# Optimization experiments

Measured on AMD Instinct MI355X. Metric: run time of the kernel, lower is better.

## Reference

```python
import jax, jax.numpy as jnp
import numpy as np

N_FFT = 1024
HOP = 256


def _hann(n):
    # torch.hann_window default is periodic
    return 0.5 * (1.0 - jnp.cos(2.0 * jnp.pi * jnp.arange(n) / n))


def _dft_kernel():
    # rfft(eye(n_fft)).T -> (n_fft//2+1, n_fft) complex, windowed along time axis
    win = _hann(N_FFT).astype(jnp.float32)
    dftm = jnp.fft.rfft(jnp.eye(N_FFT, dtype=jnp.float32), axis=-1).T * win[None, :]
    # rearrange 'f n ri -> (ri f) n': real rows first, then imag rows
    ker = jnp.concatenate([dftm.real, dftm.imag], axis=0)  # (2*(n_fft//2+1), n_fft)
    f2 = ker.shape[0]
    scale = jnp.ones((f2,), dtype=jnp.float32)
    scale = scale.at[1:(N_FFT + 1) // 2].set(2.0)   # positive freqs (real part), excl. DC & Nyquist
    scale = scale.at[(N_FFT + 2) // 2:].set(2.0)    # imag rows
    return (ker * scale[:, None] / N_FFT).astype(jnp.float32)  # (1026, 1024)


def setup_inputs() -> dict:
    key = jax.random.key(0)
    B, F, T = 16, N_FFT // 2 + 1, 1024
    x = jax.random.normal(key, (B, F, T, 2), dtype=jnp.float32)
    return {"x": x}


def reference(x) -> jnp.ndarray:
    # x: (B, freq, n_frames, 2)
    B, F, T, _ = x.shape
    # '... freq n ri -> ... (ri freq) n'
    xc = jnp.concatenate([x[..., 0], x[..., 1]], axis=1)  # (B, 2F, T)
    ker = _dft_kernel()                                   # (2F, n_fft)
    # conv_transpose1d(stride=hop) == per-frame GEMM then overlap-add
    frames = jnp.einsum('bct,cn->btn', xc, ker)           # (B, T, n_fft)
    L = (T - 1) * HOP + N_FFT
    idx = (jnp.arange(T)[:, None] * HOP + jnp.arange(N_FFT)[None, :]).reshape(-1)
    wav = jnp.zeros((B, L), dtype=x.dtype).at[:, idx].add(frames.reshape(B, -1))
    # COLA normalization: * hop / sum(window^2)
    win = _hann(N_FFT)
    coeff = (HOP / jnp.sum(win ** 2)).astype(x.dtype)
    return wav * coeff
```

## Files before the change

### kernel.cpp

```cpp
#include <hip/hip_runtime.h>
#include <hip/hip_bf16.h>

#define HOP 256
#define NB 16
#define NT 1024
#define MM (NB*NT)
#define LOUT ((NT-1)*HOP + 1024)
#define CQ (2.0f/(3.0f*1024.0f))
#define PACK_BLOCKS 2048

typedef __bf16 bf16x8 __attribute__((ext_vector_type(8)));
typedef float f32x4 __attribute__((ext_vector_type(4)));

__device__ __forceinline__ void gload_lds16(const void* g, void* l) {
  __builtin_amdgcn_global_load_lds(
      (const __attribute__((address_space(1))) void*)g,
      (__attribute__((address_space(3))) void*)l, 16, 0, 0);
}

__global__ void prep(const float* __restrict__ x, __hip_bfloat16* __restrict__ A,
                     __hip_bfloat16* __restrict__ B3, float* __restrict__ wint) {
  int tid = threadIdx.x;
  if (blockIdx.x >= PACK_BLOCKS) {
    int idx = (blockIdx.x - PACK_BLOCKS) * 256 + tid;
    int row = idx >> 9, c = idx & 511;
    int i = row & 255, nt = row >> 8;
    int oddh = i >> 7;
    int j = nt * 128 + (i & 127);
    int f, isSin;
    if (!oddh) {
      if (c < 257) { f = 2 * c; isSin = 0; } else { f = 2 * (c - 256); isSin = 1; }
    } else {
      if (c < 256) { f = 2 * c + 1; isSin = 0; } else { f = 2 * (c - 256) + 1; isSin = 1; }
    }
    const float w0 = 6.283185307179586f / 1024.f;
    int ph = (f * j) & 1023;
    float si, co;
    __sincosf((float)ph * w0, &si, &co);
    float sc = (f == 0 || f == 512) ? 1.f : 2.f;
    B3[idx] = __float2bfloat16(isSin ? -si * sc : co * sc);
    if (idx < 1024)
      wint[idx] = (0.5f - 0.5f * __cosf((float)idx * w0)) * CQ;
    return;
  }
  __shared__ float2 tile[64][65];
  int w = blockIdx.x;
  int b = w >> 7, fy = (w >> 4) & 7, tx = w & 15;
  int f0 = fy * 64, t0 = tx * 64;
  int tl = tid & 63, th = tid >> 6;
#pragma unroll
  for (int r = 0; r < 16; ++r) {
    int fl = r * 4 + th;
    tile[fl][tl] = *(const float2*)(x + (((size_t)b * 513 + f0 + fl) * 1024 + (t0 + tl)) * 2);
  }
  __syncthreads();
  int row = tid >> 2, s = tid & 3;
  float sp = 0.f;
  if (fy == 0 && s == 1)
    sp = x[(((size_t)b * 513 + 512) * 1024 + t0 + row) * 2];
  int cbase = (s & 1) * 256 + (s >> 1) * 512 + f0 / 2;
#pragma unroll
  for (int v = 0; v < 4; ++v) {
    bf16x8 pv;
#pragma unroll
    for (int u = 0; u < 8; ++u) {
      int e = v * 8 + u;
      float2 tv = tile[2 * e + (s >> 1)][row];
      float val = (s & 1) ? tv.y : tv.x;
      if (fy == 0 && s == 1 && e == 0) val = sp;
      pv[u] = (__bf16)val;
    }
    *(bf16x8*)(A + (size_t)(b * 1024 + t0 + row) * 1024 + cbase + v * 8) = pv;
  }
}

__global__ __launch_bounds__(256, 2) void gemm8(
    const __hip_bfloat16* __restrict__ A, const __hip_bfloat16* __restrict__ B3,
    const float* __restrict__ wint, __hip_bfloat16* __restrict__ C) {
  __shared__ __align__(16) __hip_bfloat16 smem[32768];
  int tid = threadIdx.x, lane = tid & 63, wv = tid >> 6;
  int wr = wv >> 1, wc = wv & 1;
  int q = blockIdx.x >> 3, xcd = blockIdx.x & 7;
  int m_ = xcd + 8 * (q >> 2);
  int nt = q & 3;
  int M0 = m_ * 128;
  int j0 = nt * 128;

  __hip_bfloat16* sA0 = smem;
  __hip_bfloat16* sA1 = smem + 8192;
  __hip_bfloat16* sB0 = smem + 16384;
  __hip_bfloat16* sB1 = smem + 24576;

  f32x4 accE[4][4] = {};
  f32x4 accO[4][4] = {};

#define SGA(KT, G, LB)                                                         \
  {                                                                            \
    int r_ = (G) * 32 + (tid >> 3);                                            \
    int s_ = (((tid & 7) ^ (r_ & 7)) * 8);                                     \
    gload_lds16(A + (size_t)(M0 + r_) * 1024 + (KT) * 64 + s_,                 \
                (LB) + (G) * 2048 + tid * 8);                                  \
  }
#define SGB(KT, G, LB)                                                         \
  {                                                                            \
    int r_ = (G) * 32 + (tid >> 3);                                            \
    int s_ = (((tid & 7) ^ (r_ & 7)) * 8);                                     \
    gload_lds16(B3 + (size_t)(nt * 256 + ((KT) >= 8 ? 128 : 0) + r_) * 512 +   \
                    ((KT) & 7) * 64 + s_,                                      \
                (LB) + (G) * 2048 + tid * 8);                                  \
  }
#define VMCNT0() asm volatile("s_waitcnt vmcnt(0)" ::: "memory")
#define BAR() __builtin_amdgcn_s_barrier()

#define TILE(CA, CB, NA, NBUF, K1, DOST, ACC)                                  \
  {                                                                            \
    if (DOST) { SGB(K1, 0, NBUF); SGB(K1, 1, NBUF);                            \
                SGB(K1, 2, NBUF); SGB(K1, 3, NBUF);                            \
                SGA(K1, 0, NA); SGA(K1, 1, NA);                                \
                SGA(K1, 2, NA); SGA(K1, 3, NA); }                              \
    bf16x8 bfr[2][4], af[4][2];                                                \
    _Pragma("unroll") for (int ni = 0; ni < 4; ++ni) {                         \
      int row = wc * 64 + ni * 16 + (lane & 15);                               \
      _Pragma("unroll") for (int ks = 0; ks < 2; ++ks)                         \
          bfr[ks][ni] = *(const bf16x8*)&(CB)[row * 64 +                       \
              (((ks * 4 + (lane >> 4)) ^ (row & 7)) * 8)];                     \
    }                                                                          \
    _Pragma("unroll") for (int mi = 0; mi < 4; ++mi) {                         \
      int row = wr * 64 + mi * 16 + (lane & 15);                               \
      _Pragma("unroll") for (int ks = 0; ks < 2; ++ks)                         \
          af[mi][ks] = *(const bf16x8*)&(CA)[row * 64 +                        \
              (((ks * 4 + (lane >> 4)) ^ (row & 7)) * 8)];                     \
    }                                                                          \
    __builtin_amdgcn_s_setprio(1);                                             \
    _Pragma("unroll") for (int mi = 0; mi < 4; ++mi)                           \
    _Pragma("unroll") for (int ks = 0; ks < 2; ++ks)                           \
    _Pragma("unroll") for (int ni = 0; ni < 4; ++ni)                           \
        ACC[mi][ni] = __builtin_amdgcn_mfma_f32_16x16x32_bf16(                 \
            af[mi][ks], bfr[ks][ni], ACC[mi][ni], 0, 0, 0);                    \
    __builtin_amdgcn_s_setprio(0);                                             \
    VMCNT0();                                                                  \
    BAR();                                                                     \
  }

  SGB(0, 0, sB0); SGB(0, 1, sB0); SGB(0, 2, sB0); SGB(0, 3, sB0);
  SGA(0, 0, sA0); SGA(0, 1, sA0); SGA(0, 2, sA0); SGA(0, 3, sA0);
  VMCNT0();
  BAR();

#pragma unroll
  for (int tt = 0; tt < 4; ++tt) {
    TILE(sA0, sB0, sA1, sB1, 2 * tt + 1, 1, accE);
    TILE(sA1, sB1, sA0, sB0, 2 * tt + 2, 1, accE);
  }
#pragma unroll
  for (int tt = 0; tt < 4; ++tt) {
    TILE(sA0, sB0, sA1, sB1, 2 * tt + 9, 1, accO);
    TILE(sA1, sB1, sA0, sB0, 2 * tt + 10, (tt < 3) ? 1 : 0, accO);
  }

  __hip_bfloat16* ct = smem;
  float wE[4], wO[4];
#pragma unroll
  for (int ni = 0; ni < 4; ++ni) {
    int jcol = j0 + wc * 64 + ni * 16 + (lane & 15);
    wE[ni] = wint[jcol];
    wO[ni] = wint[jcol + 512];
  }
#pragma unroll
  for (int mi = 0; mi < 4; ++mi) {
    int rbase = wr * 64 + mi * 16 + (lane >> 4) * 4;
#pragma unroll
    for (int ni = 0; ni < 4; ++ni) {
      int lc = wc * 64 + ni * 16 + (lane & 15);
#pragma unroll
      for (int r = 0; r < 4; ++r) {
        float E = accE[mi][ni][r], O = accO[mi][ni][r];
        ct[(rbase + r) * 256 + lc] = __float2bfloat16(wE[ni] * (E + O));
        ct[(rbase + r) * 256 + 128 + lc] = __float2bfloat16(wO[ni] * (E - O));
      }
    }
  }
  BAR();
#pragma unroll
  for (int k = 0; k < 16; ++k) {
    int row = k * 8 + (tid >> 5);
    int c0 = (tid & 31) * 8;
    int gcol = (c0 < 128) ? (j0 + c0) : (512 + j0 + c0 - 128);
    *(int4*)(C + (size_t)(M0 + row) * 1024 + gcol) = *(const int4*)&ct[row * 256 + c0];
  }
#undef SGA
#undef SGB
#undef VMCNT0
#undef BAR
#undef TILE
}

__global__ void ola2(const __hip_bfloat16* __restrict__ C, float* __restrict__ out) {
  int q = blockIdx.x;
  int b = blockIdx.y * 8 + (threadIdx.x >> 5);
  int r0 = (threadIdx.x & 31) * 8;
  size_t outl = (size_t)b * LOUT + q * 256 + r0;
  if (q >= 3 && q < 1024) {
    size_t mrow = ((size_t)b * 1024 + q) * 1024;
    bf16x8 v0 = *(const bf16x8*)&C[mrow + r0];
    bf16x8 v1 = *(const bf16x8*)&C[mrow - 1024 + 256 + r0];
    bf16x8 v2 = *(const bf16x8*)&C[mrow - 2048 + 512 + r0];
    bf16x8 v3 = *(const bf16x8*)&C[mrow - 3072 + 768 + r0];
    float res[8];
#pragma unroll
    for (int e = 0; e < 8; ++e)
      res[e] = (float)v0[e] + (float)v1[e] + (float)v2[e] + (float)v3[e];
    *(float4*)(out + outl) = make_float4(res[0], res[1], res[2], res[3]);
    *(float4*)(out + outl + 4) = make_float4(res[4], res[5], res[6], res[7]);
    return;
  }
#pragma unroll
  for (int e = 0; e < 8; ++e) {
    int l = q * 256 + r0 + e;
    int thi = l >> 8; if (thi > 1023) thi = 1023;
    int tlo = (l - 768) >> 8; if (tlo < 0) tlo = 0;
    float s = 0.f;
    for (int t = tlo; t <= thi; ++t)
      s += __bfloat162float(C[((size_t)b * 1024 + t) * 1024 + (l - (t << 8))]);
    out[outl + e] = s;
  }
}

extern "C" void kernel_launch(void* const* d_in, const int* in_sizes, int n_in,
                              void* d_out, int out_size, void* d_ws, size_t ws_size,
                              hipStream_t stream) {
  (void)in_sizes; (void)n_in; (void)out_size; (void)ws_size;
  const float* x = (const float*)d_in[0];
  float* out = (float*)d_out;
  char* ws = (char*)d_ws;
  size_t oA  = 0;
  size_t oB3 = oA + (size_t)MM * 1024 * 2;
  size_t oW  = oB3 + (size_t)1024 * 512 * 2;
  size_t oC  = oW + 1024 * 4;
  __hip_bfloat16* A  = (__hip_bfloat16*)(ws + oA);
  __hip_bfloat16* B3 = (__hip_bfloat16*)(ws + oB3);
  float* wint = (float*)(ws + oW);
  __hip_bfloat16* C  = (__hip_bfloat16*)(ws + oC);

  prep<<<dim3(PACK_BLOCKS + 2048), dim3(256), 0, stream>>>(x, A, B3, wint);
  gemm8<<<dim3(512), dim3(256), 0, stream>>>(A, B3, wint, C);
  ola2<<<dim3(1027, 2), dim3(256), 0, stream>>>(C, out);
}
```

Measured before the change: 59.45 us.

## Load B operand fragments directly from global into registers, bypassing LDS

The B (DFT kernel) tile is no longer staged through shared memory. Each wave now loads its bf16x8 MFMA fragments straight from global memory into a double-buffered register set, one tile ahead. This halves LDS traffic and removes the LDS reads for B. In exchange it adds register pressure from the second B fragment set, and each of the two column waves issues its own uncoalesced-ish global loads for the same B rows that the block previously loaded once.

```diff
diff --git a/kernel.cpp b/kernel.cpp
--- a/kernel.cpp
+++ b/kernel.cpp
@@ -88,11 +88,10 @@
 
   __hip_bfloat16* sA0 = smem;
   __hip_bfloat16* sA1 = smem + 8192;
-  __hip_bfloat16* sB0 = smem + 16384;
-  __hip_bfloat16* sB1 = smem + 24576;
 
   f32x4 accE[4][4] = {};
   f32x4 accO[4][4] = {};
+  bf16x8 bf0[2][4], bf1[2][4];
 
 #define SGA(KT, G, LB)                                                         \
   {                                                                            \
@@ -101,30 +100,22 @@
     gload_lds16(A + (size_t)(M0 + r_) * 1024 + (KT) * 64 + s_,                 \
                 (LB) + (G) * 2048 + tid * 8);                                  \
   }
-#define SGB(KT, G, LB)                                                         \
-  {                                                                            \
-    int r_ = (G) * 32 + (tid >> 3);                                            \
-    int s_ = (((tid & 7) ^ (r_ & 7)) * 8);                                     \
-    gload_lds16(B3 + (size_t)(nt * 256 + ((KT) >= 8 ? 128 : 0) + r_) * 512 +   \
-                    ((KT) & 7) * 64 + s_,                                      \
-                (LB) + (G) * 2048 + tid * 8);                                  \
+#define LOADB(DST, KT)                                                         \
+  _Pragma("unroll") for (int ni = 0; ni < 4; ++ni) {                           \
+    int brow_ = nt * 256 + (((KT) >= 8) ? 128 : 0) + wc * 64 + ni * 16 + (lane & 15); \
+    _Pragma("unroll") for (int ks = 0; ks < 2; ++ks)                           \
+        (DST)[ks][ni] = *(const bf16x8*)(B3 + (size_t)brow_ * 512 +            \
+            ((KT) & 7) * 64 + ks * 32 + (lane >> 4) * 8);                      \
   }
 #define VMCNT0() asm volatile("s_waitcnt vmcnt(0)" ::: "memory")
 #define BAR() __builtin_amdgcn_s_barrier()
 
-#define TILE(CA, CB, NA, NBUF, K1, DOST, ACC)                                  \
+#define TILE(CA, NA, K1, DOST, ACC, BC, BN)                                    \
   {                                                                            \
-    if (DOST) { SGB(K1, 0, NBUF); SGB(K1, 1, NBUF);                            \
-                SGB(K1, 2, NBUF); SGB(K1, 3, NBUF);                            \
-                SGA(K1, 0, NA); SGA(K1, 1, NA);                                \
-                SGA(K1, 2, NA); SGA(K1, 3, NA); }                              \
-    bf16x8 bfr[2][4], af[4][2];                                                \
-    _Pragma("unroll") for (int ni = 0; ni < 4; ++ni) {                         \
-      int row = wc * 64 + ni * 16 + (lane & 15);                               \
-      _Pragma("unroll") for (int ks = 0; ks < 2; ++ks)                         \
-          bfr[ks][ni] = *(const bf16x8*)&(CB)[row * 64 +                       \
-              (((ks * 4 + (lane >> 4)) ^ (row & 7)) * 8)];                     \
-    }                                                                          \
+    if (DOST) { SGA(K1, 0, NA); SGA(K1, 1, NA);                                \
+                SGA(K1, 2, NA); SGA(K1, 3, NA);                                \
+                LOADB(BN, K1); }                                               \
+    bf16x8 af[4][2];                                                           \
     _Pragma("unroll") for (int mi = 0; mi < 4; ++mi) {                         \
       int row = wr * 64 + mi * 16 + (lane & 15);                               \
       _Pragma("unroll") for (int ks = 0; ks < 2; ++ks)                         \
@@ -136,27 +127,33 @@
     _Pragma("unroll") for (int ks = 0; ks < 2; ++ks)                           \
     _Pragma("unroll") for (int ni = 0; ni < 4; ++ni)                           \
         ACC[mi][ni] = __builtin_amdgcn_mfma_f32_16x16x32_bf16(                 \
-            af[mi][ks], bfr[ks][ni], ACC[mi][ni], 0, 0, 0);                    \
+            af[mi][ks], (BC)[ks][ni], ACC[mi][ni], 0, 0, 0);                   \
     __builtin_amdgcn_s_setprio(0);                                             \
     VMCNT0();                                                                  \
     BAR();                                                                     \
   }
 
-  SGB(0, 0, sB0); SGB(0, 1, sB0); SGB(0, 2, sB0); SGB(0, 3, sB0);
   SGA(0, 0, sA0); SGA(0, 1, sA0); SGA(0, 2, sA0); SGA(0, 3, sA0);
+  LOADB(bf0, 0);
   VMCNT0();
   BAR();
 
-#pragma unroll
-  for (int tt = 0; tt < 4; ++tt) {
-    TILE(sA0, sB0, sA1, sB1, 2 * tt + 1, 1, accE);
-    TILE(sA1, sB1, sA0, sB0, 2 * tt + 2, 1, accE);
-  }
-#pragma unroll
-  for (int tt = 0; tt < 4; ++tt) {
-    TILE(sA0, sB0, sA1, sB1, 2 * tt + 9, 1, accO);
-    TILE(sA1, sB1, sA0, sB0, 2 * tt + 10, (tt < 3) ? 1 : 0, accO);
-  }
+  TILE(sA0, sA1,  1, 1, accE, bf0, bf1);
+  TILE(sA1, sA0,  2, 1, accE, bf1, bf0);
+  TILE(sA0, sA1,  3, 1, accE, bf0, bf1);
+  TILE(sA1, sA0,  4, 1, accE, bf1, bf0);
+  TILE(sA0, sA1,  5, 1, accE, bf0, bf1);
+  TILE(sA1, sA0,  6, 1, accE, bf1, bf0);
+  TILE(sA0, sA1,  7, 1, accE, bf0, bf1);
+  TILE(sA1, sA0,  8, 1, accE, bf1, bf0);
+  TILE(sA0, sA1,  9, 1, accO, bf0, bf1);
+  TILE(sA1, sA0, 10, 1, accO, bf1, bf0);
+  TILE(sA0, sA1, 11, 1, accO, bf0, bf1);
+  TILE(sA1, sA0, 12, 1, accO, bf1, bf0);
+  TILE(sA0, sA1, 13, 1, accO, bf0, bf1);
+  TILE(sA1, sA0, 14, 1, accO, bf1, bf0);
+  TILE(sA0, sA1, 15, 1, accO, bf0, bf1);
+  TILE(sA1, sA0,  0, 0, accO, bf1, bf0);
 
   __hip_bfloat16* ct = smem;
   float wE[4], wO[4];
@@ -189,7 +186,7 @@
     *(int4*)(C + (size_t)(M0 + row) * 1024 + gcol) = *(const int4*)&ct[row * 256 + c0];
   }
 #undef SGA
-#undef SGB
+#undef LOADB
 #undef VMCNT0
 #undef BAR
 #undef TILE
```

Measured after the change: 77.55 us. 30.5% more time.
